# Kernel optimization log

Hardware: AMD Instinct MI355X
Metric: run time of the kernel (lower is better)

The kernel has to match this reference:

```python
import jax, jax.numpy as jnp
import numpy as np

DIM = 384; HEADS = 12; WS = 7; SHIFT = 3
IMG_H = 56; IMG_W = 56; B = 32; MLP_HID = 1536
N = WS * WS; HEAD_DIM = DIM // HEADS


def _rel_pos_index():
    # standard Swin relative position index, shape [N, N], values in [0, (2*WS-1)^2)
    coords = np.stack(np.meshgrid(np.arange(WS), np.arange(WS), indexing='ij')).reshape(2, -1)
    rel = (coords[:, :, None] - coords[:, None, :]).transpose(1, 2, 0)
    rel[..., 0] += WS - 1
    rel[..., 1] += WS - 1
    rel[..., 0] *= 2 * WS - 1
    return jnp.asarray(rel.sum(-1))

REL_IDX = _rel_pos_index()


def _shift_mask():
    # Swin shifted-window attention mask: 0 within region, -100 across regions
    img = np.zeros((IMG_H, IMG_W))
    cnt = 0
    for hs in (slice(0, -WS), slice(-WS, -SHIFT), slice(-SHIFT, None)):
        for ws_ in (slice(0, -WS), slice(-WS, -SHIFT), slice(-SHIFT, None)):
            img[hs, ws_] = cnt
            cnt += 1
    mw = img.reshape(IMG_H // WS, WS, IMG_W // WS, WS).transpose(0, 2, 1, 3).reshape(-1, N)
    am = mw[:, None, :] - mw[:, :, None]
    return jnp.asarray(np.where(am != 0, -100.0, 0.0).astype(np.float32))


def setup_inputs() -> dict:
    key = jax.random.key(0)
    ks = jax.random.split(key, 8)
    rn = lambda k, s: jax.random.normal(k, s, jnp.float32) * 0.02
    return {
        'x': jax.random.normal(ks[0], (B, IMG_H * IMG_W, DIM), jnp.float32),
        'mask': _shift_mask(),
        'w_ln1': jnp.ones((DIM,), jnp.float32), 'b_ln1': jnp.zeros((DIM,), jnp.float32),
        'w_qkv': rn(ks[1], (3 * DIM, DIM)), 'b_qkv': jnp.zeros((3 * DIM,), jnp.float32),
        'rel_bias': rn(ks[2], ((2 * WS - 1) ** 2, HEADS)),
        'w_proj': rn(ks[3], (DIM, DIM)), 'b_proj': jnp.zeros((DIM,), jnp.float32),
        'w_ln2': jnp.ones((DIM,), jnp.float32), 'b_ln2': jnp.zeros((DIM,), jnp.float32),
        'w_fc1': rn(ks[4], (MLP_HID, DIM)), 'b_fc1': jnp.zeros((MLP_HID,), jnp.float32),
        'w_fc2': rn(ks[5], (DIM, MLP_HID)), 'b_fc2': jnp.zeros((DIM,), jnp.float32),
        'H': IMG_H, 'W': IMG_W,
    }


def _ln(x, g, b, eps=1e-5):
    mu = x.mean(-1, keepdims=True)
    var = ((x - mu) ** 2).mean(-1, keepdims=True)
    return (x - mu) * jax.lax.rsqrt(var + eps) * g + b


def reference(x, mask, w_ln1, b_ln1, w_qkv, b_qkv, rel_bias, w_proj, b_proj,
              w_ln2, b_ln2, w_fc1, b_fc1, w_fc2, b_fc2, H, W):
    Bsz, L, C = x.shape
    nW = (H // WS) * (W // WS)
    shortcut = x
    h = _ln(x, w_ln1, b_ln1).reshape(Bsz, H, W, C)
    # cyclic shift
    h = jnp.roll(h, (-SHIFT, -SHIFT), axis=(1, 2))
    # window partition -> [B*nW, N, C]
    h = h.reshape(Bsz, H // WS, WS, W // WS, WS, C).transpose(0, 1, 3, 2, 4, 5).reshape(-1, N, C)
    nB = h.shape[0]
    qkv = (h @ w_qkv.T + b_qkv).reshape(nB, N, 3, HEADS, HEAD_DIM).transpose(2, 0, 3, 1, 4)
    q, k, v = qkv[0] * (HEAD_DIM ** -0.5), qkv[1], qkv[2]  # each [nB, heads, N, hd]
    attn = jnp.einsum('bhnd,bhmd->bhnm', q, k)
    bias = rel_bias[REL_IDX].transpose(2, 0, 1)  # [heads, N, N]
    attn = attn + bias[None]
    attn = attn.reshape(Bsz, nW, HEADS, N, N) + mask[None, :, None]
    attn = jax.nn.softmax(attn, axis=-1).reshape(nB, HEADS, N, N)
    o = jnp.einsum('bhnm,bhmd->bhnd', attn, v).transpose(0, 2, 1, 3).reshape(nB, N, C)
    o = o @ w_proj.T + b_proj
    # window reverse
    o = o.reshape(Bsz, H // WS, W // WS, WS, WS, C).transpose(0, 1, 3, 2, 4, 5).reshape(Bsz, H, W, C)
    o = jnp.roll(o, (SHIFT, SHIFT), axis=(1, 2)).reshape(Bsz, H * W, C)
    x = shortcut + o
    h2 = _ln(x, w_ln2, b_ln2)
    h2 = jax.nn.gelu(h2 @ w_fc1.T + b_fc1) @ w_fc2.T + b_fc2
    return x + h2
```

## Files before the change

### kernel.cpp

```cpp
#include <hip/hip_runtime.h>
#include <stdint.h>

#define B_     32
#define IMG    56
#define L_     (IMG*IMG)
#define C_     384
#define HEADS_ 12
#define HD     32
#define WS_    7
#define N_     49
#define NWIN   64
#define NB     (B_*NWIN)
#define M_TOK  (NB*N_)
#define QKVF   1152

typedef __attribute__((ext_vector_type(8))) short bf16x8;
typedef __attribute__((ext_vector_type(4))) float f32x4;
typedef __attribute__((ext_vector_type(4))) unsigned short u16x4;

__device__ __forceinline__ float bf2f(unsigned short u) {
  union { unsigned int u; float f; } c; c.u = ((unsigned int)u) << 16; return c.f;
}
__device__ __forceinline__ unsigned short f2bf(float f) {
  union { float f; unsigned int u; } c; c.f = f;
  unsigned int r = c.u + 0x7FFFu + ((c.u >> 16) & 1u);
  return (unsigned short)(r >> 16);
}

__device__ __forceinline__ void gload_lds16(const void* g, void* l) {
  __builtin_amdgcn_global_load_lds(
      (const __attribute__((address_space(1))) unsigned int*)(uintptr_t)g,
      (__attribute__((address_space(3))) unsigned int*)(uintptr_t)l,
      16, 0, 0);
}

#define MFMA16(a, b, c) __builtin_amdgcn_mfma_f32_16x16x32_bf16((a), (b), (c), 0, 0, 0)

__global__ __launch_bounds__(256) void k_prep(
    const float* __restrict__ w_qkv, const float* __restrict__ w_proj,
    const float* __restrict__ w_fc1, const float* __restrict__ w_fc2,
    const float* __restrict__ relb,  const float* __restrict__ mask,
    ushort* __restrict__ wbq, ushort* __restrict__ wbp,
    ushort* __restrict__ wb1, ushort* __restrict__ wb2,
    ushort* __restrict__ bm)
{
  int g = blockIdx.x * 256 + threadIdx.x;
  if (g < 442368)        { wbq[g]            = f2bf(w_qkv[g]); return; }
  if (g < 589824)        { wbp[g - 442368]   = f2bf(w_proj[g - 442368]); return; }
  if (g < 1179648)       { wb1[g - 589824]   = f2bf(w_fc1[g - 589824]); return; }
  if (g < 1769472)       { wb2[g - 1179648]  = f2bf(w_fc2[g - 1179648]); return; }
  int n = g - 1769472;
  int r    = n & 3;
  int col  = (n >> 2) & 63;
  int quad = (n >> 8) & 3;
  int i    = (n >> 10) & 3;
  int hw   = n >> 12;
  int h = hw % HEADS_, wc = hw / HEADS_;
  int row = i * 16 + quad * 4 + r;
  float v;
  if (col >= N_) v = -30000.f;
  else if (row >= N_) v = 0.f;
  else {
    int idx = (row / WS_ - col / WS_ + 6) * 13 + (row % WS_ - col % WS_ + 6);
    v = relb[idx * HEADS_ + h] + mask[((size_t)wc * N_ + row) * N_ + col];
  }
  bm[n] = f2bf(v);
}

template<bool WINDOW>
__global__ __launch_bounds__(256) void k_ln(const float* __restrict__ X,
    const float* __restrict__ G, const float* __restrict__ Bb,
    ushort* __restrict__ out)
{
  int token = blockIdx.x * 4 + (threadIdx.x >> 6);
  int lane  = threadIdx.x & 63;
  const float* xp = X + (size_t)token * C_;
  float v[6];
#pragma unroll
  for (int t = 0; t < 6; t++) v[t] = xp[lane + 64*t];
  float s = 0.f, s2 = 0.f;
#pragma unroll
  for (int t = 0; t < 6; t++) { s += v[t]; s2 += v[t]*v[t]; }
#pragma unroll
  for (int off = 32; off > 0; off >>= 1) {
    s  += __shfl_down(s,  off, 64);
    s2 += __shfl_down(s2, off, 64);
  }
  s = __shfl(s, 0, 64); s2 = __shfl(s2, 0, 64);
  float mu   = s * (1.f / C_);
  float rstd = rsqrtf(s2 * (1.f / C_) - mu * mu + 1e-5f);
  size_t obase;
  if (WINDOW) {
    int b = token / L_, pix = token % L_;
    int hi = pix / IMG, wj = pix % IMG;
    int sh = hi - 3; if (sh < 0) sh += IMG;
    int sw = wj - 3; if (sw < 0) sw += IMG;
    int w = b * NWIN + (sh / WS_) * 8 + (sw / WS_);
    int p = (sh % WS_) * WS_ + (sw % WS_);
    obase = ((size_t)w * N_ + p) * C_;
  } else {
    obase = (size_t)token * C_;
  }
#pragma unroll
  for (int t = 0; t < 6; t++) {
    int c = lane + 64*t;
    out[obase + c] = f2bf((v[t] - mu) * rstd * G[c] + Bb[c]);
  }
}

template<int EPI, typename OutT>
__global__ __launch_bounds__(256, 2) void k_gemm(
    const ushort* __restrict__ A, const ushort* __restrict__ W,
    const float* __restrict__ bias, OutT* __restrict__ out,
    const float* __restrict__ res, int M, int N, int K)
{
  __shared__ __align__(16) ushort As[2][128*32];
  __shared__ __align__(16) ushort Bs[2][128*32];
  int ntn = N >> 7;
  int nwg = gridDim.x;
  int bid = (blockIdx.x & 7) * (nwg >> 3) + (blockIdx.x >> 3);
  int m0 = (bid / ntn) << 7;
  int n0 = (bid % ntn) << 7;
  int tid  = threadIdx.x;
  int wave = tid >> 6, lane = tid & 63;
  int l15  = lane & 15, quad = lane >> 4;
  int wm = (wave & 1) << 6, wn = (wave >> 1) << 6;

  int srow0 = wave * 32 + (lane >> 2);
  int srow1 = srow0 + 16;
  int scol  = (lane & 3) * 8;
  const ushort* gA0 = A + (size_t)(m0 + srow0) * K + scol;
  const ushort* gA1 = A + (size_t)(m0 + srow1) * K + scol;
  const ushort* gB0 = W + (size_t)(n0 + srow0) * K + scol;
  const ushort* gB1 = W + (size_t)(n0 + srow1) * K + scol;
  int oA0 = srow0 * 32 + scol;
  int oA1 = srow1 * 32 + scol;

  f32x4 acc[4][4];
#pragma unroll
  for (int i = 0; i < 4; i++)
#pragma unroll
    for (int j = 0; j < 4; j++) acc[i][j] = (f32x4){0.f, 0.f, 0.f, 0.f};

  gload_lds16(gA0, &As[0][oA0]);
  gload_lds16(gA1, &As[0][oA1]);
  gload_lds16(gB0, &Bs[0][oA0]);
  gload_lds16(gB1, &Bs[0][oA1]);
  gA0 += 32; gA1 += 32; gB0 += 32; gB1 += 32;
  asm volatile("s_waitcnt vmcnt(0)" : : : "memory");
  __syncthreads();

  int nt = K >> 5;
  int cur = 0;
  for (int t = 0; t < nt; t++) {
    int nxt = cur ^ 1;
    if (t + 1 < nt) {
      gload_lds16(gA0, &As[nxt][oA0]);
      gload_lds16(gA1, &As[nxt][oA1]);
      gload_lds16(gB0, &Bs[nxt][oA0]);
      gload_lds16(gB1, &Bs[nxt][oA1]);
      gA0 += 32; gA1 += 32; gB0 += 32; gB1 += 32;
    }
    bf16x8 af[4], bfr[4];
#pragma unroll
    for (int i = 0; i < 4; i++) af[i]  = *(const bf16x8*)&As[cur][(wm + i*16 + l15)*32 + quad*8];
#pragma unroll
    for (int j = 0; j < 4; j++) bfr[j] = *(const bf16x8*)&Bs[cur][(wn + j*16 + l15)*32 + quad*8];
#pragma unroll
    for (int i = 0; i < 4; i++)
#pragma unroll
      for (int j = 0; j < 4; j++)
        acc[i][j] = MFMA16(af[i], bfr[j], acc[i][j]);
    asm volatile("s_waitcnt vmcnt(0)" : : : "memory");
    __syncthreads();
    cur = nxt;
  }

  float bv[4];
#pragma unroll
  for (int j = 0; j < 4; j++) bv[j] = bias[n0 + wn + j*16 + l15];
#pragma unroll
  for (int i = 0; i < 4; i++) {
#pragma unroll
    for (int r = 0; r < 4; r++) {
      int row = m0 + wm + i*16 + quad*4 + r;
      size_t dstbase;
      if (EPI == 1) {
        int w = row / N_, p = row % N_;
        int b = w >> 6, wi = w & 63;
        int hi = (wi >> 3) * WS_ + p / WS_ + 3; if (hi >= IMG) hi -= IMG;
        int wj = (wi & 7)  * WS_ + p % WS_ + 3; if (wj >= IMG) wj -= IMG;
        dstbase = ((size_t)b * L_ + hi * IMG + wj) * C_;
      } else {
        dstbase = (size_t)row * N;
      }
#pragma unroll
      for (int j = 0; j < 4; j++) {
        int col = n0 + wn + j*16 + l15;
        float v = acc[i][j][r] + bv[j];
        if (EPI == 2) {
          float e = __expf(-1.5957691216057308f * (v + 0.044715f * v * v * v));
          v = v * __builtin_amdgcn_rcpf(1.f + e);
        }
        size_t dst = dstbase + col;
        if (EPI == 1) v += res[dst];
        if (EPI == 3) v += res[(size_t)row * N + col];
        if constexpr (sizeof(OutT) == 4) out[dst] = v;
        else                             out[dst] = f2bf(v);
      }
    }
  }
}

__global__ __launch_bounds__(256, 3) void k_attn_mfma(
    const ushort* __restrict__ qkv, const ushort* __restrict__ bm,
    ushort* __restrict__ out)
{
  __shared__ __align__(16) ushort Ps[4][64*64];
  __shared__ __align__(16) ushort Vt[4][32*64];
  int wave = threadIdx.x >> 6, lane = threadIdx.x & 63;
  int task = blockIdx.x * 4 + wave;
  int w = task / HEADS_, h = task % HEADS_;
  int l15 = lane & 15, quad = lane >> 4;

  const ushort* base = qkv + (size_t)w * N_ * QKVF + h * HD;

  bf16x8 qf[4], kf[4];
#pragma unroll
  for (int i = 0; i < 4; i++) {
    int rr = i * 16 + l15; if (rr > 48) rr = 48;
    const ushort* rp = base + (size_t)rr * QKVF + quad * 8;
    qf[i] = *(const bf16x8*)rp;
    kf[i] = *(const bf16x8*)(rp + C_);
  }

  {
    int m = lane > 48 ? 48 : lane;
    const ushort* vp = base + (size_t)m * QKVF + 2 * C_;
    bf16x8 v0 = *(const bf16x8*)vp;
    bf16x8 v1 = *(const bf16x8*)(vp + 8);
    bf16x8 v2 = *(const bf16x8*)(vp + 16);
    bf16x8 v3 = *(const bf16x8*)(vp + 24);
    ushort* vt = &Vt[wave][0];
#pragma unroll
    for (int d = 0; d < 32; d++) {
      ushort val = (ushort)(d < 8 ? v0[d & 7] : d < 16 ? v1[d & 7]
                                  : d < 24 ? v2[d & 7] : v3[d & 7]);
      vt[d * 64 + (lane ^ ((d & 7) << 3))] = val;
    }
  }

  f32x4 acc[4][4];
#pragma unroll
  for (int i = 0; i < 4; i++)
#pragma unroll
    for (int j = 0; j < 4; j++) acc[i][j] = (f32x4){0.f, 0.f, 0.f, 0.f};
#pragma unroll
  for (int i = 0; i < 4; i++)
#pragma unroll
    for (int j = 0; j < 4; j++)
      acc[i][j] = MFMA16(qf[i], kf[j], acc[i][j]);

  const ushort* bmb = bm + ((size_t)(w & 63) * HEADS_ + h) * 4096;
  float sv[4][4][4];
#pragma unroll
  for (int i = 0; i < 4; i++)
#pragma unroll
    for (int j = 0; j < 4; j++) {
      u16x4 bv = *(const u16x4*)(bmb + (((i * 4 + quad) * 64) + (j * 16 + l15)) * 4);
#pragma unroll
      for (int r = 0; r < 4; r++)
        sv[i][j][r] = acc[i][j][r] * 0.17677669529663687f + bf2f(bv[r]);
    }

  float mx[4][4], sm[4][4];
#pragma unroll
  for (int i = 0; i < 4; i++)
#pragma unroll
    for (int r = 0; r < 4; r++)
      mx[i][r] = fmaxf(fmaxf(sv[i][0][r], sv[i][1][r]),
                       fmaxf(sv[i][2][r], sv[i][3][r]));
#pragma unroll
  for (int off = 1; off <= 8; off <<= 1)
#pragma unroll
    for (int i = 0; i < 4; i++)
#pragma unroll
      for (int r = 0; r < 4; r++)
        mx[i][r] = fmaxf(mx[i][r], __shfl_xor(mx[i][r], off, 64));
#pragma unroll
  for (int i = 0; i < 4; i++)
#pragma unroll
    for (int r = 0; r < 4; r++) sm[i][r] = 0.f;
#pragma unroll
  for (int i = 0; i < 4; i++)
#pragma unroll
    for (int j = 0; j < 4; j++)
#pragma unroll
      for (int r = 0; r < 4; r++) {
        float e = __expf(sv[i][j][r] - mx[i][r]);
        sv[i][j][r] = e;
        sm[i][r] += e;
      }
#pragma unroll
  for (int off = 1; off <= 8; off <<= 1)
#pragma unroll
    for (int i = 0; i < 4; i++)
#pragma unroll
      for (int r = 0; r < 4; r++)
        sm[i][r] += __shfl_xor(sm[i][r], off, 64);

  ushort* pw = &Ps[wave][0];
#pragma unroll
  for (int i = 0; i < 4; i++)
#pragma unroll
    for (int r = 0; r < 4; r++) {
      float inv = __builtin_amdgcn_rcpf(sm[i][r]);
      int row = i * 16 + quad * 4 + r;
      int s = (row & 7) << 3;
#pragma unroll
      for (int j = 0; j < 4; j++)
        pw[row * 64 + ((j * 16 + l15) ^ s)] = f2bf(sv[i][j][r] * inv);
    }

  f32x4 o[4][2];
#pragma unroll
  for (int i = 0; i < 4; i++)
#pragma unroll
    for (int jv = 0; jv < 2; jv++) o[i][jv] = (f32x4){0.f, 0.f, 0.f, 0.f};
  const ushort* vt = &Vt[wave][0];
#pragma unroll
  for (int ks = 0; ks < 2; ks++) {
    int kc = ks * 32 + quad * 8;
    bf16x8 pa[4], vb[2];
#pragma unroll
    for (int i = 0; i < 4; i++) {
      int row = i * 16 + l15;
      pa[i] = *(const bf16x8*)&pw[row * 64 + (kc ^ ((row & 7) << 3))];
    }
#pragma unroll
    for (int jv = 0; jv < 2; jv++) {
      int nn = jv * 16 + l15;
      vb[jv] = *(const bf16x8*)&vt[nn * 64 + (kc ^ ((nn & 7) << 3))];
    }
#pragma unroll
    for (int i = 0; i < 4; i++)
#pragma unroll
      for (int jv = 0; jv < 2; jv++)
        o[i][jv] = MFMA16(pa[i], vb[jv], o[i][jv]);
  }

  ushort* op = out + ((size_t)w * N_) * C_ + h * HD;
#pragma unroll
  for (int i = 0; i < 4; i++)
#pragma unroll
    for (int r = 0; r < 4; r++) {
      int row = i * 16 + quad * 4 + r;
      if (row < N_) {
#pragma unroll
        for (int jv = 0; jv < 2; jv++)
          op[(size_t)row * C_ + jv * 16 + l15] = f2bf(o[i][jv][r]);
      }
    }
}

extern "C" void kernel_launch(void* const* d_in, const int* in_sizes, int n_in,
                              void* d_out, int out_size, void* d_ws, size_t ws_size,
                              hipStream_t stream) {
  (void)in_sizes; (void)n_in; (void)out_size; (void)ws_size;
  const float* x      = (const float*)d_in[0];
  const float* mask   = (const float*)d_in[1];
  const float* w_ln1  = (const float*)d_in[2];
  const float* b_ln1  = (const float*)d_in[3];
  const float* w_qkv  = (const float*)d_in[4];
  const float* b_qkv  = (const float*)d_in[5];
  const float* relb   = (const float*)d_in[6];
  const float* w_proj = (const float*)d_in[7];
  const float* b_proj = (const float*)d_in[8];
  const float* w_ln2  = (const float*)d_in[9];
  const float* b_ln2  = (const float*)d_in[10];
  const float* w_fc1  = (const float*)d_in[11];
  const float* b_fc1  = (const float*)d_in[12];
  const float* w_fc2  = (const float*)d_in[13];
  const float* b_fc2  = (const float*)d_in[14];

  char* ws = (char*)d_ws;
  ushort* r0 = (ushort*)ws;
  ushort* r1 = (ushort*)(ws + 308281344);
  ushort* bmt = (ushort*)(ws + 231211008);
  ushort* wbq = (ushort*)(ws + 385351680);
  ushort* wbp = wbq + QKVF * C_;
  ushort* wb1 = wbp + C_ * C_;
  ushort* wb2 = wb1 + 1536 * C_;
  float*  x1   = (float*)d_out;
  float*  outp = (float*)d_out;

  k_prep<<<4915200/256, 256, 0, stream>>>(w_qkv, w_proj, w_fc1, w_fc2,
                                          relb, mask, wbq, wbp, wb1, wb2, bmt);

  k_ln<true ><<<M_TOK/4, 256, 0, stream>>>(x, w_ln1, b_ln1, r1);
  k_gemm<0, ushort><<<(M_TOK/128)*(QKVF/128), 256, 0, stream>>>(
      r1, wbq, b_qkv, r0, nullptr, M_TOK, QKVF, 384);
  k_attn_mfma<<<NB*HEADS_/4, 256, 0, stream>>>(r0, bmt, r1);
  k_gemm<1, float><<<(M_TOK/128)*(C_/128), 256, 0, stream>>>(
      r1, wbp, b_proj, x1, x, M_TOK, C_, 384);
  k_ln<false><<<M_TOK/4, 256, 0, stream>>>(x1, w_ln2, b_ln2, r1);
  k_gemm<2, ushort><<<(M_TOK/128)*(1536/128), 256, 0, stream>>>(
      r1, wb1, b_fc1, r0, nullptr, M_TOK, 1536, 384);
  k_gemm<3, float><<<(M_TOK/128)*(C_/128), 256, 0, stream>>>(
      r0, wb2, b_fc2, outp, x1, M_TOK, C_, 1536);
}
```

Measured before the change: 1.029 ms.

## Enlarge GEMM block tile to 256x128 with 128x64 per-wave tiles

```diff
diff --git a/kernel.cpp b/kernel.cpp
--- a/kernel.cpp
+++ b/kernel.cpp
@@ -114,39 +114,38 @@
     const float* __restrict__ bias, OutT* __restrict__ out,
     const float* __restrict__ res, int M, int N, int K)
 {
-  __shared__ __align__(16) ushort As[2][128*32];
+  __shared__ __align__(16) ushort As[2][256*32];
   __shared__ __align__(16) ushort Bs[2][128*32];
   int ntn = N >> 7;
   int nwg = gridDim.x;
   int bid = (blockIdx.x & 7) * (nwg >> 3) + (blockIdx.x >> 3);
-  int m0 = (bid / ntn) << 7;
+  int m0 = (bid / ntn) << 8;
   int n0 = (bid % ntn) << 7;
   int tid  = threadIdx.x;
   int wave = tid >> 6, lane = tid & 63;
   int l15  = lane & 15, quad = lane >> 4;
-  int wm = (wave & 1) << 6, wn = (wave >> 1) << 6;
-
-  int srow0 = wave * 32 + (lane >> 2);
-  int srow1 = srow0 + 16;
-  int scol  = (lane & 3) * 8;
-  const ushort* gA0 = A + (size_t)(m0 + srow0) * K + scol;
-  const ushort* gA1 = A + (size_t)(m0 + srow1) * K + scol;
-  const ushort* gB0 = W + (size_t)(n0 + srow0) * K + scol;
-  const ushort* gB1 = W + (size_t)(n0 + srow1) * K + scol;
-  int oA0 = srow0 * 32 + scol;
-  int oA1 = srow1 * 32 + scol;
-
-  f32x4 acc[4][4];
-#pragma unroll
-  for (int i = 0; i < 4; i++)
+  int wm = (wave >> 1) << 7;
+  int wn = (wave & 1) << 6;
+
+  int srow = tid >> 2;
+  int scol = (tid & 3) * 8;
+  const ushort* gA = A + (size_t)(m0 + srow) * K + scol;
+  const ushort* gB = W + (size_t)(n0 + srow) * K + scol;
+  int oA = srow * 32 + scol;
+
+  f32x4 acc[8][4];
+#pragma unroll
+  for (int i = 0; i < 8; i++)
 #pragma unroll
     for (int j = 0; j < 4; j++) acc[i][j] = (f32x4){0.f, 0.f, 0.f, 0.f};
 
-  gload_lds16(gA0, &As[0][oA0]);
-  gload_lds16(gA1, &As[0][oA1]);
-  gload_lds16(gB0, &Bs[0][oA0]);
-  gload_lds16(gB1, &Bs[0][oA1]);
-  gA0 += 32; gA1 += 32; gB0 += 32; gB1 += 32;
+#pragma unroll
+  for (int it = 0; it < 4; it++)
+    gload_lds16(gA + (size_t)it * 64 * K, &As[0][oA + it * 2048]);
+#pragma unroll
+  for (int it = 0; it < 2; it++)
+    gload_lds16(gB + (size_t)it * 64 * K, &Bs[0][oA + it * 2048]);
+  gA += 32; gB += 32;
   asm volatile("s_waitcnt vmcnt(0)" : : : "memory");
   __syncthreads();
 
@@ -155,19 +154,21 @@
   for (int t = 0; t < nt; t++) {
     int nxt = cur ^ 1;
     if (t + 1 < nt) {
-      gload_lds16(gA0, &As[nxt][oA0]);
-      gload_lds16(gA1, &As[nxt][oA1]);
-      gload_lds16(gB0, &Bs[nxt][oA0]);
-      gload_lds16(gB1, &Bs[nxt][oA1]);
-      gA0 += 32; gA1 += 32; gB0 += 32; gB1 += 32;
-    }
-    bf16x8 af[4], bfr[4];
-#pragma unroll
-    for (int i = 0; i < 4; i++) af[i]  = *(const bf16x8*)&As[cur][(wm + i*16 + l15)*32 + quad*8];
+#pragma unroll
+      for (int it = 0; it < 4; it++)
+        gload_lds16(gA + (size_t)it * 64 * K, &As[nxt][oA + it * 2048]);
+#pragma unroll
+      for (int it = 0; it < 2; it++)
+        gload_lds16(gB + (size_t)it * 64 * K, &Bs[nxt][oA + it * 2048]);
+      gA += 32; gB += 32;
+    }
+    bf16x8 af[8], bfr[4];
+#pragma unroll
+    for (int i = 0; i < 8; i++) af[i]  = *(const bf16x8*)&As[cur][(wm + i*16 + l15)*32 + quad*8];
 #pragma unroll
     for (int j = 0; j < 4; j++) bfr[j] = *(const bf16x8*)&Bs[cur][(wn + j*16 + l15)*32 + quad*8];
 #pragma unroll
-    for (int i = 0; i < 4; i++)
+    for (int i = 0; i < 8; i++)
 #pragma unroll
       for (int j = 0; j < 4; j++)
         acc[i][j] = MFMA16(af[i], bfr[j], acc[i][j]);
@@ -180,7 +181,7 @@
 #pragma unroll
   for (int j = 0; j < 4; j++) bv[j] = bias[n0 + wn + j*16 + l15];
 #pragma unroll
-  for (int i = 0; i < 4; i++) {
+  for (int i = 0; i < 8; i++) {
 #pragma unroll
     for (int r = 0; r < 4; r++) {
       int row = m0 + wm + i*16 + quad*4 + r;
@@ -398,14 +399,14 @@
                                           relb, mask, wbq, wbp, wb1, wb2, bmt);
 
   k_ln<true ><<<M_TOK/4, 256, 0, stream>>>(x, w_ln1, b_ln1, r1);
-  k_gemm<0, ushort><<<(M_TOK/128)*(QKVF/128), 256, 0, stream>>>(
+  k_gemm<0, ushort><<<(M_TOK/256)*(QKVF/128), 256, 0, stream>>>(
       r1, wbq, b_qkv, r0, nullptr, M_TOK, QKVF, 384);
   k_attn_mfma<<<NB*HEADS_/4, 256, 0, stream>>>(r0, bmt, r1);
-  k_gemm<1, float><<<(M_TOK/128)*(C_/128), 256, 0, stream>>>(
+  k_gemm<1, float><<<(M_TOK/256)*(C_/128), 256, 0, stream>>>(
       r1, wbp, b_proj, x1, x, M_TOK, C_, 384);
   k_ln<false><<<M_TOK/4, 256, 0, stream>>>(x1, w_ln2, b_ln2, r1);
-  k_gemm<2, ushort><<<(M_TOK/128)*(1536/128), 256, 0, stream>>>(
+  k_gemm<2, ushort><<<(M_TOK/256)*(1536/128), 256, 0, stream>>>(
       r1, wb1, b_fc1, r0, nullptr, M_TOK, 1536, 384);
-  k_gemm<3, float><<<(M_TOK/128)*(C_/128), 256, 0, stream>>>(
+  k_gemm<3, float><<<(M_TOK/256)*(C_/128), 256, 0, stream>>>(
       r0, wb2, b_fc2, outp, x1, M_TOK, C_, 1536);
 }
```

Result: faster. 1.004 ms (-2.4%).
